# Optimization experiments

Hardware: AMD Instinct MI355X
Metric: run time of the kernel (lower is better)

The kernel has to match this reference:

```python
import jax, jax.numpy as jnp
import numpy as np

N_NODES = 100000
N_EDGES = 1200000
D_IN = 64
D_OUT = 64


def setup_inputs() -> dict:
    key = jax.random.key(0)
    ks = jax.random.split(key, 8)
    feat = jax.random.normal(ks[0], (N_NODES, D_IN), dtype=jnp.float32)
    src = jax.random.randint(ks[1], (N_EDGES,), 0, N_NODES, dtype=jnp.int32)
    dst = jax.random.randint(ks[2], (N_EDGES,), 0, N_NODES, dtype=jnp.int32)
    edge_weight = jax.random.uniform(ks[3], (N_EDGES, 1), dtype=jnp.float32)
    edge_mask = jax.random.uniform(ks[4], (N_EDGES, 1), dtype=jnp.float32)
    W_self = jax.random.normal(ks[5], (D_OUT, D_IN), dtype=jnp.float32) * (1.0 / np.sqrt(D_IN))
    b_self = jnp.zeros((D_OUT,), dtype=jnp.float32)
    W_neigh = jax.random.normal(ks[6], (D_OUT, D_IN), dtype=jnp.float32) * (1.0 / np.sqrt(D_IN))
    b_neigh = jnp.zeros((D_OUT,), dtype=jnp.float32)
    return {"feat": feat, "src": src, "dst": dst, "edge_weight": edge_weight,
            "edge_mask": edge_mask, "W_self": W_self, "b_self": b_self,
            "W_neigh": W_neigh, "b_neigh": b_neigh}


def reference(feat, src, dst, edge_weight, edge_mask, W_self, b_self, W_neigh, b_neigh):
    # message: gather src feats, scale by per-edge weight and mask  -> [E, D_IN]
    msg = feat[src] * edge_weight * edge_mask
    # mean scatter-reduce over incoming edges per dst node
    neigh_sum = jax.ops.segment_sum(msg, dst, num_segments=N_NODES)  # [N, D_IN]
    deg = jax.ops.segment_sum(jnp.ones((msg.shape[0],), dtype=feat.dtype), dst,
                              num_segments=N_NODES)  # [N]
    h_neigh = neigh_sum / jnp.maximum(deg, 1.0)[:, None]  # zero-degree nodes -> 0 (DGL mean semantics)
    # dual linear fuse
    rst = (feat @ W_self.T + b_self) + (h_neigh @ W_neigh.T + b_neigh)
    return rst
```

## Files before the change

### kernel.cpp

```cpp
#include <hip/hip_runtime.h>

#define NB_MAX   1568
#define CAP      1024
#define BT_EDGES 5120
#define BT_TPB   1024
#define EPE      5

typedef __attribute__((ext_vector_type(4))) float floatx4;
typedef __attribute__((ext_vector_type(2))) float floatx2;
typedef __attribute__((ext_vector_type(8))) short bf16x8;
typedef __attribute__((ext_vector_type(4))) unsigned uintx4;

__device__ __forceinline__ unsigned short f32_to_bf16(float f) {
  unsigned u = __float_as_uint(f);
  u = (u + 0x7fffu + ((u >> 16) & 1u)) >> 16;
  return (unsigned short)u;
}
__device__ __forceinline__ unsigned pack2(float a, float b) {
  return (unsigned)f32_to_bf16(a) | ((unsigned)f32_to_bf16(b) << 16);
}
__device__ __forceinline__ bf16x8 zero_bf16x8() {
  bf16x8 v;
#pragma unroll
  for (int i = 0; i < 8; ++i) v[i] = 0;
  return v;
}

#if __has_builtin(__builtin_amdgcn_cvt_pk_fp8_f32)
__device__ __forceinline__ unsigned pack_fp8x4(float a, float b, float c, float d) {
  unsigned v = (unsigned)__builtin_amdgcn_cvt_pk_fp8_f32(a, b, 0, false);
  v = (unsigned)__builtin_amdgcn_cvt_pk_fp8_f32(c, d, (int)v, true);
  return v;
}
#else
__device__ __forceinline__ unsigned sw_f32_fp8(float f) {
  unsigned u = __float_as_uint(f);
  unsigned s = (u >> 24) & 0x80u;
  unsigned au = u & 0x7fffffffu;
  if (au > 0x43E00000u) au = 0x43E00000u;
  au += 0x7FFFFu + ((au >> 20) & 1u);
  int e = (int)(au >> 23) - 120;
  if (e <= 0) return s;
  return s | ((unsigned)e << 3) | ((au >> 20) & 7u);
}
__device__ __forceinline__ unsigned pack_fp8x4(float a, float b, float c, float d) {
  return sw_f32_fp8(a) | (sw_f32_fp8(b) << 8) | (sw_f32_fp8(c) << 16) |
         (sw_f32_fp8(d) << 24);
}
#endif

#if __has_builtin(__builtin_amdgcn_cvt_pk_f32_fp8)
__device__ __forceinline__ void dec4(float* acc, unsigned w32, float wt) {
  floatx2 f0 = __builtin_amdgcn_cvt_pk_f32_fp8((int)w32, false);
  floatx2 f1 = __builtin_amdgcn_cvt_pk_f32_fp8((int)w32, true);
  acc[0] += wt * f0.x; acc[1] += wt * f0.y;
  acc[2] += wt * f1.x; acc[3] += wt * f1.y;
}
#else
__device__ __forceinline__ float sw_fp8_f32(unsigned b) {
  unsigned s = (b & 0x80u) << 24;
  unsigned e = (b >> 3) & 0xFu;
  unsigned m = b & 7u;
  float fn = __uint_as_float(s | ((e + 120u) << 23) | (m << 20));
  float fd = (float)(int)m * 0.001953125f;
  fd = (b & 0x80u) ? -fd : fd;
  return e ? fn : fd;
}
__device__ __forceinline__ void dec4(float* acc, unsigned w32, float wt) {
  acc[0] += wt * sw_fp8_f32(w32 & 0xFF);
  acc[1] += wt * sw_fp8_f32((w32 >> 8) & 0xFF);
  acc[2] += wt * sw_fp8_f32((w32 >> 16) & 0xFF);
  acc[3] += wt * sw_fp8_f32(w32 >> 24);
}
#endif

__global__ __launch_bounds__(BT_TPB) void k_build(
    const float* __restrict__ feat, const int* __restrict__ src,
    const int* __restrict__ dst, const float* __restrict__ ew,
    const float* __restrict__ em, const float* __restrict__ Ws,
    const float* __restrict__ Wn, int* __restrict__ gCursor,
    unsigned* __restrict__ recs, unsigned short* __restrict__ featb,
    unsigned char* __restrict__ featq, unsigned short* __restrict__ Wb,
    int E, int nChunks, int nB) {
  __shared__ unsigned stage[BT_EDGES];
  __shared__ unsigned short stageB[BT_EDGES];
  __shared__ int A[NB_MAX];
  __shared__ int B[NB_MAX];
  __shared__ int waveSums[16];

  const int t = threadIdx.x;
  const int lane = t & 63;
  const int wvid = t >> 6;
  const int e0 = blockIdx.x * BT_EDGES;
  const int eEnd = min(e0 + BT_EDGES, E);
  const int nLocal = eEnd - e0;

  for (int i = t; i < NB_MAX; i += BT_TPB) B[i] = 0;
  __syncthreads();

  int dreg[EPE];
  unsigned rreg[EPE];
#pragma unroll
  for (int k = 0; k < EPE; ++k) {
    int i = e0 + k * BT_TPB + t;
    dreg[k] = -1;
    if (i < eEnd) {
      int d = __builtin_nontemporal_load(&dst[i]);
      dreg[k] = d;
      atomicAdd(&B[d >> 6], 1);
      float w = __builtin_nontemporal_load(&ew[i]) *
                __builtin_nontemporal_load(&em[i]);
      int wq = (int)(w * 511.0f + 0.5f);
      if (wq > 511) wq = 511;
      rreg[k] = (unsigned)__builtin_nontemporal_load(&src[i]) |
                ((unsigned)(d & 63) << 17) | ((unsigned)wq << 23);
    }
  }
  __syncthreads();

  {
    const int EPT = 2;
    int b0 = t * EPT;
    int v[EPT];
    int sum = 0;
#pragma unroll
    for (int j = 0; j < EPT; ++j) {
      v[j] = (b0 + j < nB) ? B[b0 + j] : 0;
      sum += v[j];
    }
    int x = sum;
#pragma unroll
    for (int d = 1; d < 64; d <<= 1) {
      int y = __shfl_up(x, d, 64);
      if (lane >= d) x += y;
    }
    if (lane == 63) waveSums[wvid] = x;
    __syncthreads();
    int wprefix = 0;
    for (int i = 0; i < wvid; ++i) wprefix += waveSums[i];
    int run = wprefix + x - sum;
#pragma unroll
    for (int j = 0; j < EPT; ++j) {
      if (b0 + j < nB) A[b0 + j] = run;
      run += v[j];
    }
  }
  __syncthreads();

  for (int i = t; i < nB; i += BT_TPB) {
    int c = B[i];
    int l = A[i];
    int g = c ? atomicAdd(&gCursor[i], c) : 0;
    A[i] = i * CAP + g - l;
    B[i] = l;
  }
  __syncthreads();

#pragma unroll
  for (int k = 0; k < EPE; ++k) {
    if (dreg[k] >= 0) {
      int bkt = dreg[k] >> 6;
      int r = atomicAdd(&B[bkt], 1);
      stage[r] = rreg[k];
      stageB[r] = (unsigned short)bkt;
    }
  }
  __syncthreads();

  for (int i = t; i < nLocal; i += BT_TPB) {
    int bkt = stageB[i];
    int pos = A[bkt] + i;
    if (pos < (bkt + 1) * CAP)
      recs[pos] = stage[i];
  }

  for (int c = blockIdx.x * BT_TPB + t; c < nChunks; c += gridDim.x * BT_TPB) {
    const floatx4* fp = reinterpret_cast<const floatx4*>(feat) + (size_t)c * 2;
    floatx4 a = __builtin_nontemporal_load(fp);
    floatx4 b = __builtin_nontemporal_load(fp + 1);
    uintx4 o;
    o.x = pack2(a.x, a.y);
    o.y = pack2(a.z, a.w);
    o.z = pack2(b.x, b.y);
    o.w = pack2(b.z, b.w);
    __builtin_nontemporal_store(o, reinterpret_cast<uintx4*>(featb) + c);
    uint2 q8;
    q8.x = pack_fp8x4(a.x, a.y, a.z, a.w);
    q8.y = pack_fp8x4(b.x, b.y, b.z, b.w);
    reinterpret_cast<uint2*>(featq)[c] = q8;
  }

  if (blockIdx.x == 0) {
    for (int i = t; i < 1024; i += BT_TPB) {
      int j = i >> 4, c4 = i & 15;
      float4 w4 = reinterpret_cast<const float4*>(Ws)[i];
      float4 n4 = reinterpret_cast<const float4*>(Wn)[i];
      *reinterpret_cast<uint2*>(&Wb[j * 128 + c4 * 4]) =
          make_uint2(pack2(w4.x, w4.y), pack2(w4.z, w4.w));
      *reinterpret_cast<uint2*>(&Wb[j * 128 + 64 + c4 * 4]) =
          make_uint2(pack2(n4.x, n4.y), pack2(n4.z, n4.w));
    }
  }
}

__global__ __launch_bounds__(256, 8) void sage_gather_gemm(
    const unsigned short* __restrict__ featb,
    const unsigned char* __restrict__ featq,
    const unsigned short* __restrict__ Wb, const int* __restrict__ gCursor,
    const unsigned* __restrict__ recs, const float* __restrict__ bs,
    const float* __restrict__ bn, float* __restrict__ out, int N) {
  __shared__ unsigned short An[64][72];
  __shared__ unsigned rawL[CAP];
  __shared__ unsigned srtL[CAP];
  __shared__ int cntS[64], offS[64], curS[64];

  const int t = threadIdx.x;
  const int b = blockIdx.x;
  const int n0 = b * 64;
  const int base = b * CAP;
  const int cb = min(gCursor[b], CAP);

  if (t < 64) cntS[t] = 0;
  __syncthreads();

  for (int i = t; i < cb; i += 256) {
    unsigned r = __builtin_nontemporal_load(&recs[base + i]);
    rawL[i] = r;
    atomicAdd(&cntS[(r >> 17) & 63], 1);
  }
  __syncthreads();

  if (t < 64) {
    int c = cntS[t];
    int x = c;
#pragma unroll
    for (int d = 1; d < 64; d <<= 1) {
      int y = __shfl_up(x, d, 64);
      if (t >= d) x += y;
    }
    offS[t] = x - c;
    curS[t] = x - c;
  }
  __syncthreads();

  for (int i = t; i < cb; i += 256) {
    unsigned r = rawL[i];
    int p = atomicAdd(&curS[(r >> 17) & 63], 1);
    srtL[p] = r;
  }
  __syncthreads();

  const int wv = t >> 6;
  const int ln = t & 63;
  const int col = ln & 15;
  const int quad = ln >> 4;
  const int gn = n0 + wv * 16 + col;
  bf16x8 af0 = zero_bf16x8(), af1 = zero_bf16x8();

  {
    const int nl = t >> 2;
    const int q  = t & 3;
    const int deg = cntS[nl], off = offS[nl];
    float acc[16];
#pragma unroll
    for (int i = 0; i < 16; ++i) acc[i] = 0.f;
    const uint4* fq = reinterpret_cast<const uint4*>(featq);

    uint4 uC = {0, 0, 0, 0}, uN = {0, 0, 0, 0};
    float wC = 0.f, wN = 0.f;
    if (deg > 0) {
      unsigned r0 = srtL[off];
      uC = fq[(size_t)(r0 & 0x1FFFF) * 4 + q];
      wC = (float)(r0 >> 23) * (1.0f / 511.0f);
    }
    if (deg > 1) {
      unsigned r1 = srtL[off + 1];
      uN = fq[(size_t)(r1 & 0x1FFFF) * 4 + q];
      wN = (float)(r1 >> 23) * (1.0f / 511.0f);
    }
    for (int m = 0; m < deg; ++m) {
      uint4 u = uC;
      float w = wC;
      uC = uN; wC = wN;
      if (m + 2 < deg) {
        unsigned rn = srtL[off + m + 2];
        uN = fq[(size_t)(rn & 0x1FFFF) * 4 + q];
        wN = (float)(rn >> 23) * (1.0f / 511.0f);
      }
      dec4(acc + 0, u.x, w);
      dec4(acc + 4, u.y, w);
      dec4(acc + 8, u.z, w);
      dec4(acc + 12, u.w, w);
    }

    float inv = 1.0f / fmaxf((float)deg, 1.0f);
#pragma unroll
    for (int i = 0; i < 16; ++i) acc[i] *= inv;
    uint4 o0, o1;
    o0.x = pack2(acc[0], acc[1]);
    o0.y = pack2(acc[2], acc[3]);
    o0.z = pack2(acc[4], acc[5]);
    o0.w = pack2(acc[6], acc[7]);
    o1.x = pack2(acc[8], acc[9]);
    o1.y = pack2(acc[10], acc[11]);
    o1.z = pack2(acc[12], acc[13]);
    o1.w = pack2(acc[14], acc[15]);
    *reinterpret_cast<uint4*>(&An[nl][q * 16]) = o0;
    *reinterpret_cast<uint4*>(&An[nl][q * 16 + 8]) = o1;
  }

  if (gn < N) {
    af0 = __builtin_nontemporal_load(
        reinterpret_cast<const bf16x8*>(featb + (size_t)gn * 64 + quad * 8));
    af1 = __builtin_nontemporal_load(
        reinterpret_cast<const bf16x8*>(featb + (size_t)gn * 64 + 32 + quad * 8));
  }
  floatx4 acc4[4];
#pragma unroll
  for (int jt = 0; jt < 4; ++jt) {
    float bb = bs[jt * 16 + col] + bn[jt * 16 + col];
    acc4[jt] = (floatx4){bb, bb, bb, bb};
  }
  __syncthreads();

#pragma unroll
  for (int kk = 0; kk < 4; ++kk) {
    bf16x8 af;
    if (kk == 0)      af = af0;
    else if (kk == 1) af = af1;
    else
      af = *reinterpret_cast<const bf16x8*>(
          &An[wv * 16 + col][(kk - 2) * 32 + quad * 8]);
#pragma unroll
    for (int jt = 0; jt < 4; ++jt) {
      bf16x8 bf = *reinterpret_cast<const bf16x8*>(
          Wb + (jt * 16 + col) * 128 + kk * 32 + quad * 8);
      acc4[jt] = __builtin_amdgcn_mfma_f32_16x16x32_bf16(af, bf, acc4[jt], 0, 0, 0);
    }
  }

#pragma unroll
  for (int jt = 0; jt < 4; ++jt) {
#pragma unroll
    for (int r = 0; r < 4; ++r) {
      int m = quad * 4 + r;
      int g2 = n0 + wv * 16 + m;
      if (g2 < N)
        __builtin_nontemporal_store(acc4[jt][r],
                                    &out[(size_t)g2 * 64 + jt * 16 + col]);
    }
  }
}

extern "C" void kernel_launch(void* const* d_in, const int* in_sizes, int n_in,
                              void* d_out, int out_size, void* d_ws, size_t ws_size,
                              hipStream_t stream) {
  const float* feat = (const float*)d_in[0];
  const int*   src  = (const int*)d_in[1];
  const int*   dst  = (const int*)d_in[2];
  const float* ew   = (const float*)d_in[3];
  const float* em   = (const float*)d_in[4];
  const float* Ws   = (const float*)d_in[5];
  const float* bs   = (const float*)d_in[6];
  const float* Wn   = (const float*)d_in[7];
  const float* bn   = (const float*)d_in[8];
  float* out = (float*)d_out;

  const int N = in_sizes[0] / 64;
  const int E = in_sizes[1];
  const int nB = (N + 63) / 64;

  unsigned short* featb = (unsigned short*)d_ws;
  unsigned char*  featq = (unsigned char*)(featb + (size_t)N * 64);
  unsigned short* Wb    = (unsigned short*)(featq + (size_t)N * 64);
  unsigned* recs   = (unsigned*)(Wb + 64 * 128);
  int*      gCursor = (int*)(recs + (size_t)NB_MAX * CAP);

  hipMemsetAsync(gCursor, 0, NB_MAX * sizeof(int), stream);

  int nChunks = N * 8;
  int gB = (E + BT_EDGES - 1) / BT_EDGES;

  k_build<<<gB, BT_TPB, 0, stream>>>(feat, src, dst, ew, em, Ws, Wn,
                                     gCursor, recs, featb, featq, Wb,
                                     E, nChunks, nB);
  sage_gather_gemm<<<nB, 256, 0, stream>>>(featb, featq, Wb, gCursor, recs,
                                           bs, bn, out, N);
}
```

Baseline: 155.5 us.

## Split FP8 feature table into two half-planes and gather in two passes

The FP8 quantized feature table is stored as two planes, each holding 32 of the 64 columns, so every row in a plane is 32 bytes instead of 64. The neighbour gather now runs twice, once per plane, with 8-byte loads per lane. The aim is a smaller per-pass working set and better cache locality for the random gather. In exchange the src records in LDS are read twice, and the accumulated columns go into the An tile in a different column order that the GEMM must still consume correctly.

```diff
diff --git a/kernel.cpp b/kernel.cpp
--- a/kernel.cpp
+++ b/kernel.cpp
@@ -174,6 +174,7 @@
       recs[pos] = stage[i];
   }
 
+  const size_t PL = (size_t)nChunks * 4;
   for (int c = blockIdx.x * BT_TPB + t; c < nChunks; c += gridDim.x * BT_TPB) {
     const floatx4* fp = reinterpret_cast<const floatx4*>(feat) + (size_t)c * 2;
     floatx4 a = __builtin_nontemporal_load(fp);
@@ -187,7 +188,8 @@
     uint2 q8;
     q8.x = pack_fp8x4(a.x, a.y, a.z, a.w);
     q8.y = pack_fp8x4(b.x, b.y, b.z, b.w);
-    reinterpret_cast<uint2*>(featq)[c] = q8;
+    int n = c >> 3, h = (c >> 2) & 1, j = c & 3;
+    reinterpret_cast<uint2*>(featq + (size_t)h * PL)[(size_t)n * 4 + j] = q8;
   }
 
   if (blockIdx.x == 0) {
@@ -264,34 +266,40 @@
     float acc[16];
 #pragma unroll
     for (int i = 0; i < 16; ++i) acc[i] = 0.f;
-    const uint4* fq = reinterpret_cast<const uint4*>(featq);
-
-    uint4 uC = {0, 0, 0, 0}, uN = {0, 0, 0, 0};
-    float wC = 0.f, wN = 0.f;
-    if (deg > 0) {
-      unsigned r0 = srtL[off];
-      uC = fq[(size_t)(r0 & 0x1FFFF) * 4 + q];
-      wC = (float)(r0 >> 23) * (1.0f / 511.0f);
-    }
-    if (deg > 1) {
-      unsigned r1 = srtL[off + 1];
-      uN = fq[(size_t)(r1 & 0x1FFFF) * 4 + q];
-      wN = (float)(r1 >> 23) * (1.0f / 511.0f);
-    }
-    for (int m = 0; m < deg; ++m) {
-      uint4 u = uC;
-      float w = wC;
-      uC = uN; wC = wN;
-      if (m + 2 < deg) {
-        unsigned rn = srtL[off + m + 2];
-        uN = fq[(size_t)(rn & 0x1FFFF) * 4 + q];
-        wN = (float)(rn >> 23) * (1.0f / 511.0f);
-      }
-      dec4(acc + 0, u.x, w);
-      dec4(acc + 4, u.y, w);
-      dec4(acc + 8, u.z, w);
-      dec4(acc + 12, u.w, w);
-    }
+    const uint2* fq0 = reinterpret_cast<const uint2*>(featq);
+    const uint2* fq1 =
+        reinterpret_cast<const uint2*>(featq + (size_t)N * 32);
+
+#define GPHASE(FQ, A0, A1)                                   \
+    {                                                        \
+      uint2 uC = {0, 0}, uN = {0, 0};                        \
+      float wC = 0.f, wN = 0.f;                              \
+      if (deg > 0) {                                         \
+        unsigned r0 = srtL[off];                             \
+        uC = FQ[(size_t)(r0 & 0x1FFFF) * 4 + q];             \
+        wC = (float)(r0 >> 23) * (1.0f / 511.0f);            \
+      }                                                      \
+      if (deg > 1) {                                         \
+        unsigned r1 = srtL[off + 1];                         \
+        uN = FQ[(size_t)(r1 & 0x1FFFF) * 4 + q];             \
+        wN = (float)(r1 >> 23) * (1.0f / 511.0f);            \
+      }                                                      \
+      for (int m = 0; m < deg; ++m) {                        \
+        uint2 u = uC;                                        \
+        float w = wC;                                        \
+        uC = uN; wC = wN;                                    \
+        if (m + 2 < deg) {                                   \
+          unsigned rn = srtL[off + m + 2];                   \
+          uN = FQ[(size_t)(rn & 0x1FFFF) * 4 + q];           \
+          wN = (float)(rn >> 23) * (1.0f / 511.0f);          \
+        }                                                    \
+        dec4(acc + (A0), u.x, w);                            \
+        dec4(acc + (A1), u.y, w);                            \
+      }                                                      \
+    }
+    GPHASE(fq0, 0, 4)
+    GPHASE(fq1, 8, 12)
+#undef GPHASE
 
     float inv = 1.0f / fmaxf((float)deg, 1.0f);
 #pragma unroll
@@ -305,8 +313,8 @@
     o1.y = pack2(acc[10], acc[11]);
     o1.z = pack2(acc[12], acc[13]);
     o1.w = pack2(acc[14], acc[15]);
-    *reinterpret_cast<uint4*>(&An[nl][q * 16]) = o0;
-    *reinterpret_cast<uint4*>(&An[nl][q * 16 + 8]) = o1;
+    *reinterpret_cast<uint4*>(&An[nl][q * 8]) = o0;
+    *reinterpret_cast<uint4*>(&An[nl][32 + q * 8]) = o1;
   }
 
   if (gn < N) {
```

Result: slower. 162.7 us (+4.6%).
